# Performance work log

Measured on AMD Instinct MI355X. Metric: run time of the kernel, lower is better.

The kernel has to match this reference:

```python
import jax, jax.numpy as jnp
import numpy as np

L = 2        # n_layers
F = 128      # in_features == out_features (GRUCell + highway constraint)
O = 128
N = 1024     # nodes
B = 8        # batch
D = 3        # edge directions (weight.size(0))


def setup_inputs() -> dict:
    key = jax.random.key(0)
    ks = jax.random.split(key, 10)
    s = 1.0 / np.sqrt(F)
    u = lambda k, shp: jax.random.uniform(k, shp, jnp.float32, minval=-s, maxval=s)
    return {
        "inputs": jax.random.normal(ks[0], (N, B, F), jnp.float32),
        "adj": jax.random.uniform(ks[1], (D, B, N, N), jnp.float32),
        "W": u(ks[2], (L, D, F, O)),            # GCN weight per layer/direction
        "Bc": u(ks[3], (L, D, O)),              # GCN bias
        "Wh": u(ks[4], (L, F, O)),              # highway weight
        "Bh": u(ks[5], (L, O)),                 # highway bias
        "Wih": u(ks[6], (L, 3 * O, O)),         # GRUCell input weights
        "Whh": u(ks[7], (L, 3 * O, O)),         # GRUCell hidden weights
        "bih": u(ks[8], (L, 3 * O)),
        "bhh": u(ks[9], (L, 3 * O)),
    }


def _gru(x, h, wih, whh, bih, bhh):
    # torch.nn.GRUCell semantics; x,h: [..., O]
    gi = x @ wih.T + bih
    gh = h @ whh.T + bhh
    i_r, i_z, i_n = jnp.split(gi, 3, axis=-1)
    h_r, h_z, h_n = jnp.split(gh, 3, axis=-1)
    r = jax.nn.sigmoid(i_r + h_r)
    z = jax.nn.sigmoid(i_z + h_z)
    n = jnp.tanh(i_n + r * h_n)
    return (1.0 - z) * n + z * h


def reference(inputs, adj, W, Bc, Wh, Bh, Wih, Whh, bih, bhh):
    x = inputs  # [N, B, F]; dropout layers are identity at eval
    for l in range(L):
        # support per direction: [D, B, N, O]
        support = jnp.einsum('nbf,dfo->dbno', x, W[l]) + Bc[l][:, None, None, :]
        # adjacency-weighted aggregation: adj[d,b] @ support[d,b]
        agg = jnp.einsum('dbmn,dbno->dbmo', adj, support)
        # GRU update with hidden = current features, per direction, summed over d
        h = jnp.broadcast_to(jnp.transpose(x, (1, 0, 2))[None], agg.shape)
        hnew = _gru(agg, h, Wih[l], Whh[l], bih[l], bhh[l])
        out = jnp.transpose(jnp.sum(hnew, axis=0), (1, 0, 2))  # [N, B, O]
        out = jax.nn.relu(out)  # activation='relu'
        # highway gate (highway='relu')
        t = jax.nn.relu(jnp.einsum('nbf,fo->nbo', x, Wh[l]) + Bh[l])
        x = out * t + x * (1.0 - t)
    return x
```

## Files before the change

### kernel.cpp

```cpp
#include <hip/hip_runtime.h>
#include <math.h>

#define N_NODES 1024
#define BATCH   8
#define FEAT    128
#define NDIR    3
#define NB      (N_NODES*BATCH)
#define G3      384

typedef __bf16 bf16_t;
using bf16x8 = __attribute__((ext_vector_type(8))) __bf16;
using bf16x4 = __attribute__((ext_vector_type(4))) __bf16;
using f32x4  = __attribute__((ext_vector_type(4))) float;

#define GLOAD_LDS16(g, l) \
    __builtin_amdgcn_global_load_lds((const __attribute__((address_space(1))) void*)(g), \
                                     (__attribute__((address_space(3))) void*)(l), 16, 0, 0)

#define STAGE64(As, Bs, Arow, Brow, sA, sB, k0, w, lane)                      \
    {                                                                          \
        _Pragma("unroll")                                                      \
        for (int q = 0; q < 2; ++q) {                                          \
            int qq = (w)*2 + q;                                                \
            int row = qq*8 + ((lane) >> 3), seg = (lane) & 7;                  \
            GLOAD_LDS16((Arow) + (size_t)row*(sA) + (k0) + seg*8,              \
                        (char*)(As) + qq*1024);                                \
            GLOAD_LDS16((Brow) + (size_t)row*(sB) + (k0) + seg*8,              \
                        (char*)(Bs) + qq*1024);                                \
        }                                                                      \
    }

#define MFMA64(As, Bs, acc, w, lane)                                           \
    {                                                                          \
        _Pragma("unroll")                                                      \
        for (int ks = 0; ks < 64; ks += 32) {                                  \
            bf16x8 af = *reinterpret_cast<const bf16x8*>(                      \
                &(As)[((w)*16 + ((lane) & 15))*64 + ks + (((lane) >> 4) * 8)]);\
            _Pragma("unroll")                                                  \
            for (int j = 0; j < 4; ++j) {                                      \
                bf16x8 bfv = *reinterpret_cast<const bf16x8*>(                 \
                    &(Bs)[(j*16 + ((lane) & 15))*64 + ks + (((lane) >> 4) * 8)]);\
                (acc)[j] = __builtin_amdgcn_mfma_f32_16x16x32_bf16(af, bfv, (acc)[j], 0, 0, 0); \
            }                                                                  \
        }                                                                      \
    }

__global__ __launch_bounds__(256) void k_cvt_adj(
    const float* __restrict__ src, bf16_t* __restrict__ dst, int n4)
{
    int i = blockIdx.x * 256 + threadIdx.x;
    int stride = gridDim.x * 256;
    for (; i < n4; i += stride) {
        float4 v = reinterpret_cast<const float4*>(src)[i];
        bf16x4 o;
        o[0] = (bf16_t)(v.x - 0.5f); o[1] = (bf16_t)(v.y - 0.5f);
        o[2] = (bf16_t)(v.z - 0.5f); o[3] = (bf16_t)(v.w - 0.5f);
        *reinterpret_cast<bf16x4*>(&dst[(size_t)i * 4]) = o;
    }
}

__global__ __launch_bounds__(128) void k_wprep(
    const float* __restrict__ W, const float* __restrict__ Wh,
    const float* __restrict__ Whh, const float* __restrict__ Wih,
    bf16_t* __restrict__ wsup,
    bf16_t* __restrict__ whhc,
    bf16_t* __restrict__ wihc)
{
    int m = blockIdx.x, l = blockIdx.y, k = threadIdx.x;
    float w;
    bf16_t* dst;
    bool patB = false;
    if (m < 384) {
        int d = m >> 7, o = m & 127;
        w = W[((size_t)(l*3 + d)*128 + k)*128 + o];
        dst = wsup + ((size_t)l*512 + m)*384;
    } else if (m < 512) {
        int o = m - 384;
        w = Wh[((size_t)l*128 + k)*128 + o];
        dst = wsup + ((size_t)l*512 + m)*384;
    } else if (m < 896) {
        int c = m - 512;
        w = Whh[((size_t)l*384 + c)*128 + k];
        dst = whhc + ((size_t)l*384 + c)*384;
    } else {
        int c = m - 896;
        w = Wih[((size_t)l*384 + c)*128 + k];
        dst = wihc + ((size_t)l*384 + c)*384;
        patB = true;
    }
    bf16_t hi = (bf16_t)w;
    bf16_t lo = (bf16_t)(w - (float)hi);
    if (patB) { dst[k] = hi; dst[128 + k] = hi; dst[256 + k] = lo; }
    else      { dst[k] = hi; dst[128 + k] = lo; dst[256 + k] = hi; }
}

__global__ __launch_bounds__(256) void k_xcat(
    const float* __restrict__ X, bf16_t* __restrict__ xcat)
{
    int idx = blockIdx.x * 256 + threadIdx.x;
    int k = idx & 127, r = idx >> 7;
    int n = r >> 3, b = r & 7;
    float v = X[idx];
    bf16_t hi = (bf16_t)v;
    bf16_t lo = (bf16_t)(v - (float)hi);
    bf16_t* dst = xcat + ((size_t)(b*1024 + n))*384 + k;
    dst[0] = hi; dst[128] = hi; dst[256] = lo;
}

__global__ __launch_bounds__(256, 4) void k_sup(
    const bf16_t* __restrict__ Wcat,
    const bf16_t* __restrict__ xcat,
    const float* __restrict__ Bcl,
    const float* __restrict__ Bhl,
    bf16_t* __restrict__ supt,
    float* __restrict__ tbuf)
{
    __shared__ bf16_t As[64*64];
    __shared__ bf16_t Bs[64*64];
    const int t = threadIdx.x, lane = t & 63, w = t >> 6;
    const int n0 = blockIdx.x * 64;
    const int m0 = blockIdx.y * 64;
    const int b  = blockIdx.z;
    const bf16_t* Arow = Wcat + (size_t)m0 * 384;
    const bf16_t* Brow = xcat + ((size_t)b * 1024 + n0) * 384;

    f32x4 acc[4] = {};
    for (int k0 = 0; k0 < 384; k0 += 64) {
        STAGE64(As, Bs, Arow, Brow, 384, 384, k0, w, lane);
        __syncthreads();
        MFMA64(As, Bs, acc, w, lane);
        __syncthreads();
    }
    #pragma unroll
    for (int j = 0; j < 4; ++j) {
        int n = n0 + j*16 + (lane & 15);
        #pragma unroll
        for (int rg = 0; rg < 4; ++rg) {
            int m = m0 + w*16 + (lane >> 4)*4 + rg;
            float v = acc[j][rg];
            if (m < 384) {
                int d = m >> 7, o = m & 127;
                supt[((size_t)((d*8 + b)*128 + o))*1024 + n] = (bf16_t)(v + Bcl[d*128 + o]);
            } else {
                int o = m - 384;
                tbuf[((size_t)(b*128 + o))*1024 + n] = fmaxf(v + Bhl[o], 0.0f);
            }
        }
    }
}

__global__ __launch_bounds__(256) void k_colsum(
    const bf16_t* __restrict__ supt, float* __restrict__ colsum)
{
    int row = blockIdx.x * 4 + (threadIdx.x >> 6);
    int lane = threadIdx.x & 63;
    const bf16_t* p = supt + (size_t)row * 1024 + lane * 16;
    bf16x8 v0 = *reinterpret_cast<const bf16x8*>(p);
    bf16x8 v1 = *reinterpret_cast<const bf16x8*>(p + 8);
    float s = 0.0f;
    #pragma unroll
    for (int i = 0; i < 8; ++i) s += (float)v0[i] + (float)v1[i];
    #pragma unroll
    for (int off = 32; off > 0; off >>= 1) s += __shfl_down(s, off, 64);
    if (lane == 0) colsum[row] = s;
}

__global__ __launch_bounds__(256, 4) void k_gh(
    const bf16_t* __restrict__ A,
    const bf16_t* __restrict__ B,
    const float* __restrict__ bias,
    bf16_t* __restrict__ C)
{
    __shared__ bf16_t As[64*64];
    __shared__ bf16_t Bs[64*64];
    const int t = threadIdx.x, lane = t & 63, w = t >> 6;
    const int m0 = blockIdx.x * 64;
    const int c0 = blockIdx.y * 64;
    const bf16_t* Arow = A + (size_t)m0 * 384;
    const bf16_t* Brow = B + (size_t)c0 * 384;

    f32x4 acc[4] = {};
    for (int k0 = 0; k0 < 384; k0 += 64) {
        STAGE64(As, Bs, Arow, Brow, 384, 384, k0, w, lane);
        __syncthreads();
        MFMA64(As, Bs, acc, w, lane);
        __syncthreads();
    }
    #pragma unroll
    for (int j = 0; j < 4; ++j) {
        int c = c0 + j*16 + (lane & 15);
        float bv = bias[c];
        #pragma unroll
        for (int rg = 0; rg < 4; ++rg) {
            int m = m0 + w*16 + (lane >> 4)*4 + rg;
            C[(size_t)m*G3 + c] = (bf16_t)(acc[j][rg] + bv);
        }
    }
}

__global__ __launch_bounds__(256, 4) void k_agg(
    const bf16_t* __restrict__ adjb,
    const bf16_t* __restrict__ supt,
    const float* __restrict__ colsum,
    bf16_t* __restrict__ aggcat)
{
    __shared__ bf16_t As[64*64];
    __shared__ bf16_t Bs[64*64];
    const int t = threadIdx.x, lane = t & 63, w = t >> 6;
    const int m0 = blockIdx.x * 64;
    const int o0 = blockIdx.y * 64;
    const int z  = blockIdx.z;
    const bf16_t* Arow = adjb + (size_t)z * 1024 * 1024 + (size_t)m0 * 1024;
    const bf16_t* Brow = supt + (size_t)z * 128 * 1024 + (size_t)o0 * 1024;

    f32x4 acc[4] = {};
    for (int k0 = 0; k0 < 1024; k0 += 64) {
        STAGE64(As, Bs, Arow, Brow, 1024, 1024, k0, w, lane);
        __syncthreads();
        MFMA64(As, Bs, acc, w, lane);
        __syncthreads();
    }
    #pragma unroll
    for (int j = 0; j < 4; ++j) {
        int o = o0 + j*16 + (lane & 15);
        float cs = 0.5f * colsum[z*128 + o];
        #pragma unroll
        for (int rg = 0; rg < 4; ++rg) {
            size_t m = (size_t)z*1024 + m0 + w*16 + (lane >> 4)*4 + rg;
            float v = acc[j][rg] + cs;
            bf16_t hi = (bf16_t)v;
            bf16_t lo = (bf16_t)(v - (float)hi);
            bf16_t* row = aggcat + m*384;
            row[o] = hi; row[128 + o] = lo; row[256 + o] = hi;
        }
    }
}

__global__ __launch_bounds__(256, 4) void k_gi(
    const bf16_t* __restrict__ A,
    const bf16_t* __restrict__ B,
    const float*  __restrict__ bias,
    bf16_t* __restrict__ girz,
    float* __restrict__ gin)
{
    __shared__ bf16_t As[64*64];
    __shared__ bf16_t Bs[64*64];
    const int t = threadIdx.x, lane = t & 63, w = t >> 6;
    const int m0 = blockIdx.x * 64;
    const int c0 = blockIdx.y * 64;
    const bf16_t* Arow = A + (size_t)m0 * 384;
    const bf16_t* Brow = B + (size_t)c0 * 384;

    f32x4 acc[4] = {};
    for (int k0 = 0; k0 < 384; k0 += 64) {
        STAGE64(As, Bs, Arow, Brow, 384, 384, k0, w, lane);
        __syncthreads();
        MFMA64(As, Bs, acc, w, lane);
        __syncthreads();
    }
    #pragma unroll
    for (int j = 0; j < 4; ++j) {
        int c = c0 + j*16 + (lane & 15);
        float bv = bias[c];
        #pragma unroll
        for (int rg = 0; rg < 4; ++rg) {
            int m = m0 + w*16 + (lane >> 4)*4 + rg;
            float v = acc[j][rg] + bv;
            if (c < 256) girz[(size_t)m*256 + c] = (bf16_t)v;
            else         gin[(size_t)m*128 + (c - 256)] = v;
        }
    }
}

__global__ __launch_bounds__(256) void k_gates(
    const bf16_t* __restrict__ girz, const float* __restrict__ gin,
    const bf16_t* __restrict__ ghb,
    bf16_t* xcat,
    const float* __restrict__ tbuf,
    float* __restrict__ Xout, int write_xcat)
{
    __shared__ float ts[128*17];
    const int b = blockIdx.y, n0 = blockIdx.x * 16;
    const int tid = threadIdx.x;
    {
        int o = tid >> 1, nh = (tid & 1) * 8;
        const float* src = tbuf + ((size_t)(b*128 + o))*1024 + n0 + nh;
        float4 v0 = *reinterpret_cast<const float4*>(src);
        float4 v1 = *reinterpret_cast<const float4*>(src + 4);
        float* dst = &ts[o*17 + nh];
        dst[0]=v0.x; dst[1]=v0.y; dst[2]=v0.z; dst[3]=v0.w;
        dst[4]=v1.x; dst[5]=v1.y; dst[6]=v1.z; dst[7]=v1.w;
    }
    __syncthreads();
    #pragma unroll
    for (int p = 0; p < 8; ++p) {
        int e = p*256 + tid;
        int nn = e >> 7, o = e & 127;
        int n = n0 + nn;
        size_t rb = (size_t)(b*1024 + n);
        bf16_t* xr = xcat + rb*384;
        float h = (float)xr[o] + (float)xr[256 + o];
        const bf16_t* ghr = ghb + rb*G3;
        float g_r = (float)ghr[o], g_z = (float)ghr[128+o], g_n = (float)ghr[256+o];
        float acc = 0.0f;
        #pragma unroll
        for (int d = 0; d < 3; ++d) {
            size_t rr = (size_t)((d*8 + b)*1024 + n);
            float i_r = (float)girz[rr*256 + o];
            float i_z = (float)girz[rr*256 + 128 + o];
            float i_n = gin[rr*128 + o];
            float rg = 1.0f / (1.0f + expf(-(i_r + g_r)));
            float zg = 1.0f / (1.0f + expf(-(i_z + g_z)));
            float ng = tanhf(i_n + rg * g_n);
            acc += (1.0f - zg) * ng + zg * h;
        }
        float outv = fmaxf(acc, 0.0f);
        float tg = ts[o*17 + nn];
        float res = outv * tg + h * (1.0f - tg);
        if (Xout) Xout[(size_t)(n*8 + b)*128 + o] = res;
        if (write_xcat) {
            bf16_t hi = (bf16_t)res;
            bf16_t lo = (bf16_t)(res - (float)hi);
            xr[o] = hi; xr[128 + o] = hi; xr[256 + o] = lo;
        }
    }
}

extern "C" void kernel_launch(void* const* d_in, const int* in_sizes, int n_in,
                              void* d_out, int out_size, void* d_ws, size_t ws_size,
                              hipStream_t stream) {
    const float* inputs = (const float*)d_in[0];
    const float* adj    = (const float*)d_in[1];
    const float* W      = (const float*)d_in[2];
    const float* Bc     = (const float*)d_in[3];
    const float* Wh     = (const float*)d_in[4];
    const float* Bh     = (const float*)d_in[5];
    const float* Wih    = (const float*)d_in[6];
    const float* Whh    = (const float*)d_in[7];
    const float* bih    = (const float*)d_in[8];
    const float* bhh    = (const float*)d_in[9];

    char* ws = (char*)d_ws;
    float*  tbuf   = (float*)ws;   ws += (size_t)8*128*1024*4;
    bf16_t* xcat   = (bf16_t*)ws;  ws += (size_t)8*1024*384*2;
    bf16_t* ghb    = (bf16_t*)ws;  ws += (size_t)NB*G3*2;
    bf16_t* supt   = (bf16_t*)ws;  ws += (size_t)24*128*1024*2;
    bf16_t* aggcat = (bf16_t*)ws;  ws += (size_t)3*NB*384*2;
    bf16_t* girz   = (bf16_t*)ws;  ws += (size_t)3*NB*256*2;
    float*  gin    = (float*)ws;   ws += (size_t)3*NB*128*4;
    float*  colsum = (float*)ws;   ws += (size_t)24*128*4;
    bf16_t* wsup   = (bf16_t*)ws;  ws += (size_t)2*512*384*2;
    bf16_t* whhc   = (bf16_t*)ws;  ws += (size_t)2*384*384*2;
    bf16_t* wihc   = (bf16_t*)ws;  ws += (size_t)2*384*384*2;
    bf16_t* adjb   = (bf16_t*)ws;

    k_cvt_adj<<<dim3(4096), dim3(256), 0, stream>>>(adj, adjb, 3*8*1024*1024/4);
    k_wprep<<<dim3(1280, 2), dim3(128), 0, stream>>>(W, Wh, Whh, Wih, wsup, whhc, wihc);
    k_xcat<<<dim3(4096), dim3(256), 0, stream>>>(inputs, xcat);

    for (int l = 0; l < 2; ++l) {
        k_sup<<<dim3(16, 8, 8), dim3(256), 0, stream>>>(
            wsup + (size_t)l*512*384, xcat, Bc + l*3*128, Bh + l*128, supt, tbuf);
        k_colsum<<<dim3(768), dim3(256), 0, stream>>>(supt, colsum);
        k_gh<<<dim3(128, 6), dim3(256), 0, stream>>>(
            xcat, whhc + (size_t)l*384*384, bhh + l*G3, ghb);
        k_agg<<<dim3(16, 2, 24), dim3(256), 0, stream>>>(adjb, supt, colsum, aggcat);
        k_gi<<<dim3(384, 6), dim3(256), 0, stream>>>(
            aggcat, wihc + (size_t)l*384*384, bih + l*G3, girz, gin);
        k_gates<<<dim3(64, 8), dim3(256), 0, stream>>>(
            girz, gin, ghb, xcat, tbuf,
            (l == 1) ? (float*)d_out : (float*)nullptr, (l == 0) ? 1 : 0);
    }
}
```

Baseline: 344.3 us.

## Fuse sup/gh GEMMs, compute colsum algebraically, widen agg tile to 128 outputs

Merges the support and hidden-gate GEMMs into one launch with a flat grid so they share the GPU. Replaces the separate column-sum pass over supt with an algebraic form: the sum of x over nodes, projected by W and bias, with x sums produced by the gates kernel through atomics. The aggregation GEMM now covers all 128 output columns per block, so each adjacency tile is loaded once instead of twice. This trades higher per-block LDS and register use for less adjacency traffic and fewer launches, and the algebraic colsum is computed in fp32 from x rather than from bf16 support values.

```diff
diff --git a/kernel.cpp b/kernel.cpp
--- a/kernel.cpp
+++ b/kernel.cpp
@@ -107,22 +107,50 @@
     dst[0] = hi; dst[128] = hi; dst[256] = lo;
 }
 
-__global__ __launch_bounds__(256, 4) void k_sup(
+__global__ __launch_bounds__(256) void k_xsum0(
+    const float* __restrict__ X, float* __restrict__ xsum)
+{
+    __shared__ float red[256];
+    int b = blockIdx.x, t = threadIdx.x;
+    int o = t & 127, h = t >> 7;
+    float s = 0.0f;
+    for (int n = h; n < 1024; n += 2)
+        s += X[(size_t)(n*8 + b)*128 + o];
+    red[t] = s;
+    __syncthreads();
+    if (t < 128) {
+        xsum[b*128 + t] = red[t] + red[t + 128];
+        xsum[1024 + b*128 + t] = 0.0f;
+    }
+}
+
+__global__ __launch_bounds__(256, 4) void k_supgh(
     const bf16_t* __restrict__ Wcat,
     const bf16_t* __restrict__ xcat,
+    const bf16_t* __restrict__ whhc,
     const float* __restrict__ Bcl,
     const float* __restrict__ Bhl,
+    const float* __restrict__ bhh,
     bf16_t* __restrict__ supt,
-    float* __restrict__ tbuf)
+    float* __restrict__ tbuf,
+    bf16_t* __restrict__ ghb)
 {
     __shared__ bf16_t As[64*64];
     __shared__ bf16_t Bs[64*64];
     const int t = threadIdx.x, lane = t & 63, w = t >> 6;
-    const int n0 = blockIdx.x * 64;
-    const int m0 = blockIdx.y * 64;
-    const int b  = blockIdx.z;
-    const bf16_t* Arow = Wcat + (size_t)m0 * 384;
-    const bf16_t* Brow = xcat + ((size_t)b * 1024 + n0) * 384;
+    const int id = blockIdx.x;
+    const bf16_t *Arow, *Brow;
+    int m0, n0 = 0, b = 0, c0 = 0;
+    if (id < 1024) {
+        n0 = (id & 15) * 64; m0 = ((id >> 4) & 7) * 64; b = id >> 7;
+        Arow = Wcat + (size_t)m0 * 384;
+        Brow = xcat + ((size_t)b * 1024 + n0) * 384;
+    } else {
+        int g = id - 1024;
+        m0 = (g & 127) * 64; c0 = (g >> 7) * 64;
+        Arow = xcat + (size_t)m0 * 384;
+        Brow = whhc + (size_t)c0 * 384;
+    }
 
     f32x4 acc[4] = {};
     for (int k0 = 0; k0 < 384; k0 += 64) {
@@ -131,45 +159,122 @@
         MFMA64(As, Bs, acc, w, lane);
         __syncthreads();
     }
+    if (id < 1024) {
+        #pragma unroll
+        for (int j = 0; j < 4; ++j) {
+            int n = n0 + j*16 + (lane & 15);
+            #pragma unroll
+            for (int rg = 0; rg < 4; ++rg) {
+                int m = m0 + w*16 + (lane >> 4)*4 + rg;
+                float v = acc[j][rg];
+                if (m < 384) {
+                    int d = m >> 7, o = m & 127;
+                    supt[((size_t)((d*8 + b)*128 + o))*1024 + n] = (bf16_t)(v + Bcl[d*128 + o]);
+                } else {
+                    int o = m - 384;
+                    tbuf[((size_t)(b*128 + o))*1024 + n] = fmaxf(v + Bhl[o], 0.0f);
+                }
+            }
+        }
+    } else {
+        #pragma unroll
+        for (int j = 0; j < 4; ++j) {
+            int c = c0 + j*16 + (lane & 15);
+            float bv = bhh[c];
+            #pragma unroll
+            for (int rg = 0; rg < 4; ++rg) {
+                int m = m0 + w*16 + (lane >> 4)*4 + rg;
+                ghb[(size_t)m*G3 + c] = (bf16_t)(acc[j][rg] + bv);
+            }
+        }
+    }
+}
+
+__global__ __launch_bounds__(256, 4) void k_agg(
+    const bf16_t* __restrict__ adjb,
+    const bf16_t* __restrict__ supt,
+    const float* __restrict__ xsum,
+    const float* __restrict__ Wl,
+    const float* __restrict__ Bcl,
+    bf16_t* __restrict__ aggcat)
+{
+    __shared__ bf16_t As[64*64];
+    __shared__ bf16_t Bs[128*64];
+    __shared__ float xs[128];
+    __shared__ float red[256];
+    __shared__ float cs_sh[128];
+    const int t = threadIdx.x, lane = t & 63, w = t >> 6;
+    const int m0 = blockIdx.x * 64;
+    const int z  = blockIdx.y;
+    const int b  = z & 7, d = z >> 3;
+
+    if (t < 128) xs[t] = xsum[b*128 + t];
+    __syncthreads();
+    {
+        int o = t & 127, h = t >> 7;
+        float s = 0.0f;
+        const float* Wd = Wl + (size_t)d*128*128;
+        for (int k = h*64; k < h*64 + 64; ++k)
+            s += xs[k] * Wd[k*128 + o];
+        red[t] = s;
+        __syncthreads();
+        if (t < 128)
+            cs_sh[t] = 0.5f*(red[t] + red[t+128]) + 512.0f*Bcl[d*128 + t];
+        __syncthreads();
+    }
+
+    const bf16_t* Az = adjb + (size_t)z*1024*1024 + (size_t)m0*1024;
+    const bf16_t* Bz = supt + (size_t)z*128*1024;
+
+    f32x4 acc[8] = {};
+    for (int k0 = 0; k0 < 1024; k0 += 64) {
+        #pragma unroll
+        for (int q = 0; q < 6; ++q) {
+            int c = w*6 + q;
+            int rl = (lane >> 3), seg = (lane & 7)*8;
+            if (c < 8)
+                GLOAD_LDS16(Az + (size_t)(c*8 + rl)*1024 + k0 + seg,
+                            (char*)As + c*1024);
+            else
+                GLOAD_LDS16(Bz + (size_t)((c-8)*8 + rl)*1024 + k0 + seg,
+                            (char*)Bs + (c-8)*1024);
+        }
+        __syncthreads();
+        #pragma unroll
+        for (int ks = 0; ks < 64; ks += 32) {
+            bf16x8 af = *reinterpret_cast<const bf16x8*>(
+                &As[(w*16 + (lane & 15))*64 + ks + ((lane >> 4)*8)]);
+            #pragma unroll
+            for (int j = 0; j < 8; ++j) {
+                bf16x8 bfv = *reinterpret_cast<const bf16x8*>(
+                    &Bs[(j*16 + (lane & 15))*64 + ks + ((lane >> 4)*8)]);
+                acc[j] = __builtin_amdgcn_mfma_f32_16x16x32_bf16(af, bfv, acc[j], 0, 0, 0);
+            }
+        }
+        __syncthreads();
+    }
     #pragma unroll
-    for (int j = 0; j < 4; ++j) {
-        int n = n0 + j*16 + (lane & 15);
+    for (int j = 0; j < 8; ++j) {
+        int o = j*16 + (lane & 15);
+        float cs = cs_sh[o];
         #pragma unroll
         for (int rg = 0; rg < 4; ++rg) {
-            int m = m0 + w*16 + (lane >> 4)*4 + rg;
-            float v = acc[j][rg];
-            if (m < 384) {
-                int d = m >> 7, o = m & 127;
-                supt[((size_t)((d*8 + b)*128 + o))*1024 + n] = (bf16_t)(v + Bcl[d*128 + o]);
-            } else {
-                int o = m - 384;
-                tbuf[((size_t)(b*128 + o))*1024 + n] = fmaxf(v + Bhl[o], 0.0f);
-            }
-        }
-    }
-}
-
-__global__ __launch_bounds__(256) void k_colsum(
-    const bf16_t* __restrict__ supt, float* __restrict__ colsum)
-{
-    int row = blockIdx.x * 4 + (threadIdx.x >> 6);
-    int lane = threadIdx.x & 63;
-    const bf16_t* p = supt + (size_t)row * 1024 + lane * 16;
-    bf16x8 v0 = *reinterpret_cast<const bf16x8*>(p);
-    bf16x8 v1 = *reinterpret_cast<const bf16x8*>(p + 8);
-    float s = 0.0f;
-    #pragma unroll
-    for (int i = 0; i < 8; ++i) s += (float)v0[i] + (float)v1[i];
-    #pragma unroll
-    for (int off = 32; off > 0; off >>= 1) s += __shfl_down(s, off, 64);
-    if (lane == 0) colsum[row] = s;
-}
-
-__global__ __launch_bounds__(256, 4) void k_gh(
+            size_t m = (size_t)z*1024 + m0 + w*16 + (lane >> 4)*4 + rg;
+            float v = acc[j][rg] + cs;
+            bf16_t hi = (bf16_t)v;
+            bf16_t lo = (bf16_t)(v - (float)hi);
+            bf16_t* row = aggcat + m*384;
+            row[o] = hi; row[128 + o] = lo; row[256 + o] = hi;
+        }
+    }
+}
+
+__global__ __launch_bounds__(256, 4) void k_gi(
     const bf16_t* __restrict__ A,
     const bf16_t* __restrict__ B,
-    const float* __restrict__ bias,
-    bf16_t* __restrict__ C)
+    const float*  __restrict__ bias,
+    bf16_t* __restrict__ girz,
+    float* __restrict__ gin)
 {
     __shared__ bf16_t As[64*64];
     __shared__ bf16_t Bs[64*64];
@@ -193,78 +298,6 @@
         #pragma unroll
         for (int rg = 0; rg < 4; ++rg) {
             int m = m0 + w*16 + (lane >> 4)*4 + rg;
-            C[(size_t)m*G3 + c] = (bf16_t)(acc[j][rg] + bv);
-        }
-    }
-}
-
-__global__ __launch_bounds__(256, 4) void k_agg(
-    const bf16_t* __restrict__ adjb,
-    const bf16_t* __restrict__ supt,
-    const float* __restrict__ colsum,
-    bf16_t* __restrict__ aggcat)
-{
-    __shared__ bf16_t As[64*64];
-    __shared__ bf16_t Bs[64*64];
-    const int t = threadIdx.x, lane = t & 63, w = t >> 6;
-    const int m0 = blockIdx.x * 64;
-    const int o0 = blockIdx.y * 64;
-    const int z  = blockIdx.z;
-    const bf16_t* Arow = adjb + (size_t)z * 1024 * 1024 + (size_t)m0 * 1024;
-    const bf16_t* Brow = supt + (size_t)z * 128 * 1024 + (size_t)o0 * 1024;
-
-    f32x4 acc[4] = {};
-    for (int k0 = 0; k0 < 1024; k0 += 64) {
-        STAGE64(As, Bs, Arow, Brow, 1024, 1024, k0, w, lane);
-        __syncthreads();
-        MFMA64(As, Bs, acc, w, lane);
-        __syncthreads();
-    }
-    #pragma unroll
-    for (int j = 0; j < 4; ++j) {
-        int o = o0 + j*16 + (lane & 15);
-        float cs = 0.5f * colsum[z*128 + o];
-        #pragma unroll
-        for (int rg = 0; rg < 4; ++rg) {
-            size_t m = (size_t)z*1024 + m0 + w*16 + (lane >> 4)*4 + rg;
-            float v = acc[j][rg] + cs;
-            bf16_t hi = (bf16_t)v;
-            bf16_t lo = (bf16_t)(v - (float)hi);
-            bf16_t* row = aggcat + m*384;
-            row[o] = hi; row[128 + o] = lo; row[256 + o] = hi;
-        }
-    }
-}
-
-__global__ __launch_bounds__(256, 4) void k_gi(
-    const bf16_t* __restrict__ A,
-    const bf16_t* __restrict__ B,
-    const float*  __restrict__ bias,
-    bf16_t* __restrict__ girz,
-    float* __restrict__ gin)
-{
-    __shared__ bf16_t As[64*64];
-    __shared__ bf16_t Bs[64*64];
-    const int t = threadIdx.x, lane = t & 63, w = t >> 6;
-    const int m0 = blockIdx.x * 64;
-    const int c0 = blockIdx.y * 64;
-    const bf16_t* Arow = A + (size_t)m0 * 384;
-    const bf16_t* Brow = B + (size_t)c0 * 384;
-
-    f32x4 acc[4] = {};
-    for (int k0 = 0; k0 < 384; k0 += 64) {
-        STAGE64(As, Bs, Arow, Brow, 384, 384, k0, w, lane);
-        __syncthreads();
-        MFMA64(As, Bs, acc, w, lane);
-        __syncthreads();
-    }
-    #pragma unroll
-    for (int j = 0; j < 4; ++j) {
-        int c = c0 + j*16 + (lane & 15);
-        float bv = bias[c];
-        #pragma unroll
-        for (int rg = 0; rg < 4; ++rg) {
-            int m = m0 + w*16 + (lane >> 4)*4 + rg;
             float v = acc[j][rg] + bv;
             if (c < 256) girz[(size_t)m*256 + c] = (bf16_t)v;
             else         gin[(size_t)m*128 + (c - 256)] = v;
@@ -277,9 +310,11 @@
     const bf16_t* __restrict__ ghb,
     bf16_t* xcat,
     const float* __restrict__ tbuf,
-    float* __restrict__ Xout, int write_xcat)
+    float* __restrict__ Xout, int write_xcat,
+    float* __restrict__ xsum_next)
 {
     __shared__ float ts[128*17];
+    __shared__ float red[256];
     const int b = blockIdx.y, n0 = blockIdx.x * 16;
     const int tid = threadIdx.x;
     {
@@ -292,6 +327,7 @@
         dst[4]=v1.x; dst[5]=v1.y; dst[6]=v1.z; dst[7]=v1.w;
     }
     __syncthreads();
+    float xacc = 0.0f;
     #pragma unroll
     for (int p = 0; p < 8; ++p) {
         int e = p*256 + tid;
@@ -317,12 +353,19 @@
         float outv = fmaxf(acc, 0.0f);
         float tg = ts[o*17 + nn];
         float res = outv * tg + h * (1.0f - tg);
+        xacc += res;
         if (Xout) Xout[(size_t)(n*8 + b)*128 + o] = res;
         if (write_xcat) {
             bf16_t hi = (bf16_t)res;
             bf16_t lo = (bf16_t)(res - (float)hi);
             xr[o] = hi; xr[128 + o] = hi; xr[256 + o] = lo;
         }
+    }
+    if (xsum_next) {
+        red[tid] = xacc;
+        __syncthreads();
+        if (tid < 128)
+            atomicAdd(xsum_next + b*128 + tid, red[tid] + red[tid + 128]);
     }
 }
 
@@ -348,7 +391,7 @@
     bf16_t* aggcat = (bf16_t*)ws;  ws += (size_t)3*NB*384*2;
     bf16_t* girz   = (bf16_t*)ws;  ws += (size_t)3*NB*256*2;
     float*  gin    = (float*)ws;   ws += (size_t)3*NB*128*4;
-    float*  colsum = (float*)ws;   ws += (size_t)24*128*4;
+    float*  xsum   = (float*)ws;   ws += (size_t)2*8*128*4;
     bf16_t* wsup   = (bf16_t*)ws;  ws += (size_t)2*512*384*2;
     bf16_t* whhc   = (bf16_t*)ws;  ws += (size_t)2*384*384*2;
     bf16_t* wihc   = (bf16_t*)ws;  ws += (size_t)2*384*384*2;
@@ -357,18 +400,20 @@
     k_cvt_adj<<<dim3(4096), dim3(256), 0, stream>>>(adj, adjb, 3*8*1024*1024/4);
     k_wprep<<<dim3(1280, 2), dim3(128), 0, stream>>>(W, Wh, Whh, Wih, wsup, whhc, wihc);
     k_xcat<<<dim3(4096), dim3(256), 0, stream>>>(inputs, xcat);
+    k_xsum0<<<dim3(8), dim3(256), 0, stream>>>(inputs, xsum);
 
     for (int l = 0; l < 2; ++l) {
-        k_sup<<<dim3(16, 8, 8), dim3(256), 0, stream>>>(
-            wsup + (size_t)l*512*384, xcat, Bc + l*3*128, Bh + l*128, supt, tbuf);
-        k_colsum<<<dim3(768), dim3(256), 0, stream>>>(supt, colsum);
-        k_gh<<<dim3(128, 6), dim3(256), 0, stream>>>(
-            xcat, whhc + (size_t)l*384*384, bhh + l*G3, ghb);
-        k_agg<<<dim3(16, 2, 24), dim3(256), 0, stream>>>(adjb, supt, colsum, aggcat);
+        k_supgh<<<dim3(1792), dim3(256), 0, stream>>>(
+            wsup + (size_t)l*512*384, xcat, whhc + (size_t)l*384*384,
+            Bc + l*3*128, Bh + l*128, bhh + l*G3, supt, tbuf, ghb);
+        k_agg<<<dim3(16, 24), dim3(256), 0, stream>>>(
+            adjb, supt, xsum + l*1024, W + (size_t)l*3*128*128, Bc + l*3*128,
+            aggcat);
         k_gi<<<dim3(384, 6), dim3(256), 0, stream>>>(
             aggcat, wihc + (size_t)l*384*384, bih + l*G3, girz, gin);
         k_gates<<<dim3(64, 8), dim3(256), 0, stream>>>(
             girz, gin, ghb, xcat, tbuf,
-            (l == 1) ? (float*)d_out : (float*)nullptr, (l == 0) ? 1 : 0);
-    }
-}
+            (l == 1) ? (float*)d_out : (float*)nullptr, (l == 0) ? 1 : 0,
+            (l == 0) ? (xsum + 1024) : (float*)nullptr);
+    }
+}
```

Measured after the change: 473.6 us. +37.6%, slower.
